# Optimization experiments

Hardware: AMD Instinct MI355X
Metric: run time of the kernel (lower is better)

Reference implementation:

```python
import jax, jax.numpy as jnp
import numpy as np

LBASE = 256
L1_BASE = LBASE // 2 + 1   # 129
LPA = 128
L1_PA = LPA + 1            # 129
L2 = 16
L2_HALF = L2 // 2          # 8
L3 = 64
LOUTPUT = L3 + LPA + LBASE // 2  # 320
MAX_PLY = 60
COUNT = 6
BUCKET_SIZE = MAX_PLY // COUNT   # 10
B = 262144


def setup_inputs() -> dict:
    key = jax.random.key(0)
    ks = jax.random.split(key, 12)
    def w(k, shape, fan_in):
        bound = 1.0 / np.sqrt(fan_in)
        return jax.random.uniform(k, shape, jnp.float32, -bound, bound)
    return {
        "x_base": jax.random.uniform(ks[0], (B, LBASE // 2), jnp.float32),
        "x_pa": jax.random.uniform(ks[1], (B, LPA), jnp.float32),
        "mobility": jax.random.uniform(ks[2], (B, 1), jnp.float32),
        "ply": jax.random.randint(ks[3], (B,), 0, MAX_PLY),
        "W1b": w(ks[4], (COUNT, L2_HALF, L1_BASE), L1_BASE),
        "b1b": w(ks[5], (COUNT, L2_HALF), L1_BASE),
        "W1pa": w(ks[6], (COUNT, L2_HALF, L1_PA), L1_PA),
        "b1pa": w(ks[7], (COUNT, L2_HALF), L1_PA),
        "W2": w(ks[8], (COUNT, L3, L2 * 2), L2 * 2),
        "b2": w(ks[9], (COUNT, L3), L2 * 2),
        "Wout": w(ks[10], (COUNT, 1, LOUTPUT), LOUTPUT),
        "bout": jnp.zeros((COUNT, 1), jnp.float32),  # bias zeroed in __init__
    }


def _stacked_linear(x, W, b, idx):
    # per-sample bucket selection: x (B,I), W (C,O,I), b (C,O), idx (B,)
    return jnp.einsum("bi,boi->bo", x, W[idx]) + b[idx]


def reference(x_base, x_pa, mobility, ply, W1b, b1b, W1pa, b1pa, W2, b2, Wout, bout):
    idx = ply // BUCKET_SIZE                                   # (B,)
    mob = jnp.minimum(mobility * (7.0 / 255.0), 1.0)           # clamp max only
    xb = jnp.concatenate([x_base, mob], axis=1)                # (B,129)
    xpa = jnp.concatenate([x_pa, mob], axis=1)                 # (B,129)
    l1 = jnp.concatenate([
        _stacked_linear(xb, W1b, b1b, idx),
        _stacked_linear(xpa, W1pa, b1pa, idx),
    ], axis=1)                                                 # (B,16)
    l1_sq = jnp.square(l1) * (255.0 / 256.0)
    l1c = jnp.clip(jnp.concatenate([l1_sq, l1], axis=1), 0.0, 1.0)  # (B,32)
    l2x = _stacked_linear(l1c, W2, b2, idx)                    # (B,64)
    l2x = jnp.square(jnp.clip(l2x, 0.0, 1.0)) * (255.0 / 256.0)
    feats = jnp.concatenate([l2x, x_base, x_pa], axis=1)       # (B,320)
    return _stacked_linear(feats, Wout, bout, idx)             # (B,1)
```

## Files before the change

kernel.cpp:

```cpp
#include <hip/hip_runtime.h>


#define NB 6
#define BT 512
#define NW (BT / 64)

typedef _Float16 h2 __attribute__((ext_vector_type(2)));
typedef _Float16 h8 __attribute__((ext_vector_type(8)));
typedef float f4 __attribute__((ext_vector_type(4)));

__device__ __forceinline__ h2 pk2(float x, float y) {
    return __builtin_bit_cast(h2, __builtin_amdgcn_cvt_pkrtz(x, y));
}

__device__ __forceinline__ h8 pack8(const float4 a, const float4 b) {
    h2 p0 = pk2(a.x, a.y), p1 = pk2(a.z, a.w);
    h2 p2 = pk2(b.x, b.y), p3 = pk2(b.z, b.w);
    h8 r;
    r[0] = p0[0]; r[1] = p0[1]; r[2] = p1[0]; r[3] = p1[1];
    r[4] = p2[0]; r[5] = p2[1]; r[6] = p3[0]; r[7] = p3[1];
    return r;
}

__device__ __forceinline__ float actv(float v) {
    float u = fminf(fmaxf(v, 0.0f), 1.0f);
    return u * u * (255.0f / 256.0f);
}

__global__ __launch_bounds__(BT, 4)
void layerstacks_mfma(const float* __restrict__ x_base,
                      const float* __restrict__ x_pa,
                      const float* __restrict__ mobility,
                      const int*   __restrict__ ply,
                      const float* __restrict__ W1b,
                      const float* __restrict__ b1b,
                      const float* __restrict__ W1pa,
                      const float* __restrict__ b1pa,
                      const float* __restrict__ W2,
                      const float* __restrict__ b2,
                      const float* __restrict__ Wout,
                      const float* __restrict__ bout,
                      float* __restrict__ out)
{
    __shared__ __align__(16) _Float16 sW1[NB][2][4][4][9][8];
    __shared__ __align__(16) _Float16 sW2[NB][4][4][16][8];
    __shared__ float sWo0[NB][64];
    __shared__ float sB2[NB][64];
    __shared__ float sB1[NB][4][8];
    __shared__ float sBout[NB];
    __shared__ float sMob[BT];
    __shared__ int   sList[BT + NB * 16];
    __shared__ __align__(16) char sL1[NW * 1280];
    __shared__ int sCnt[8], sCur[8], sTb[40];
    __shared__ int sNt;

    const int tid   = threadIdx.x;
    const int lane  = tid & 63;
    const int w     = tid >> 6;
    const int gbase = blockIdx.x * BT;

    if (tid < 8) { sCnt[tid] = 0; }

    for (int e = tid; e < NB * 2 * 4 * 4 * 9 * 8; e += BT) {
        int i = e & 7;
        int rest = e >> 3;
        int n = rest % 9;   rest /= 9;
        int kb = rest & 3;  rest >>= 2;
        int t = rest & 3;   rest >>= 2;
        int st = rest & 1;
        int b = rest >> 1;
        int k = t * 32 + kb * 8 + i;
        float v;
        if (n < 8) {
            const float* Wx = st ? W1pa : W1b;
            v = Wx[b * 1032 + n * 129 + k];
        } else {
            v = st ? Wout[b * 320 + 192 + k] : Wout[b * 320 + 64 + k];
        }
        sW1[b][st][t][kb][n][i] = (_Float16)v;
    }
    for (int e = tid; e < NB * 4 * 4 * 16 * 8; e += BT) {
        int i = e & 7;
        int j = (e >> 3) & 15;
        int kb = (e >> 7) & 3;
        int T = (e >> 9) & 3;
        int b = e >> 11;
        int n = T * 16 + j;
        int k = kb * 8 + i;
        int u = k >> 1;
        int colw = (k & 1) ? (16 + u) : u;
        sW2[b][T][kb][j][i] = (_Float16)W2[b * 2048 + n * 32 + colw];
    }
    for (int e = tid; e < NB * 64; e += BT) {
        int b = e >> 6, n = e & 63;
        sWo0[b][n] = Wout[b * 320 + n];
        sB2[b][n]  = b2[e];
    }
    if (tid < NB * 4 * 8) {
        int n = tid & 7, which = (tid >> 3) & 3, b = tid >> 5;
        float v;
        if (which == 0)      v = b1b[b * 8 + n];
        else if (which == 1) v = b1pa[b * 8 + n];
        else if (which == 2) v = W1b [b * 1032 + n * 129 + 128];
        else                 v = W1pa[b * 1032 + n * 129 + 128];
        sB1[b][which][n] = v;
    }
    if (tid < NB) sBout[tid] = bout[tid];
    sMob[tid] = fminf(mobility[gbase + tid] * (7.0f / 255.0f), 1.0f);
    for (int e = tid; e < BT + NB * 16; e += BT) sList[e] = -1;

    const int bb = ply[gbase + tid] / 10;
    __syncthreads();

    #pragma unroll
    for (int b = 0; b < NB; ++b) {
        unsigned long long mk = __ballot(bb == b);
        if (bb == b) {
            int lead = __ffsll((long long)mk) - 1;
            if (lane == lead) atomicAdd(&sCnt[b], __popcll(mk));
        }
    }
    __syncthreads();

    if (tid == 0) {
        int off = 0, tt = 0;
        for (int b = 0; b < NB; ++b) {
            sCur[b] = off;
            int ntl = (sCnt[b] + 15) >> 4;
            for (int q = 0; q < ntl; ++q) sTb[tt++] = b;
            off += ntl << 4;
        }
        sNt = tt;
    }
    __syncthreads();

    #pragma unroll
    for (int b = 0; b < NB; ++b) {
        unsigned long long mk = __ballot(bb == b);
        if (bb == b) {
            int lead = __ffsll((long long)mk) - 1;
            int pfx = __popcll(mk & ((1ull << lane) - 1ull));
            int base = 0;
            if (lane == lead) base = atomicAdd(&sCur[b], __popcll(mk));
            base = __shfl(base, lead);
            sList[base + pfx] = tid;
        }
    }
    __syncthreads();

    const int ntiles = sNt;
    const int col = lane & 15;
    const int qd  = lane >> 4;
    char* lb = sL1 + w * 1280;

    for (int tl = w; tl < ntiles; tl += NW) {
        const int bkt = sTb[tl];
        const int t16 = tl << 4;

        const int sl0 = sList[t16 + qd * 4 + 0];
        const int sl1 = sList[t16 + qd * 4 + 1];
        const int sl2 = sList[t16 + qd * 4 + 2];
        const int sl3 = sList[t16 + qd * 4 + 3];
        int sA = sList[t16 + col];
        if (sA < 0) sA = sList[t16];

        const float* xbrow = x_base + (size_t)(gbase + sA) * 128 + qd * 8;
        const float* xprow = x_pa   + (size_t)(gbase + sA) * 128 + qd * 8;

        float4 b00, b01, b10, b11, b20, b21, b30, b31;
        float4 q00, q01, q10, q11, q20, q21, q30, q31;
        asm volatile(
            "global_load_dwordx4 %0,  %[ab], off\n\t"
            "global_load_dwordx4 %1,  %[ab], off offset:16\n\t"
            "global_load_dwordx4 %2,  %[ab], off offset:128\n\t"
            "global_load_dwordx4 %3,  %[ab], off offset:144\n\t"
            "global_load_dwordx4 %4,  %[ab], off offset:256\n\t"
            "global_load_dwordx4 %5,  %[ab], off offset:272\n\t"
            "global_load_dwordx4 %6,  %[ab], off offset:384\n\t"
            "global_load_dwordx4 %7,  %[ab], off offset:400\n\t"
            "global_load_dwordx4 %8,  %[ap], off\n\t"
            "global_load_dwordx4 %9,  %[ap], off offset:16\n\t"
            "global_load_dwordx4 %10, %[ap], off offset:128\n\t"
            "global_load_dwordx4 %11, %[ap], off offset:144\n\t"
            "global_load_dwordx4 %12, %[ap], off offset:256\n\t"
            "global_load_dwordx4 %13, %[ap], off offset:272\n\t"
            "global_load_dwordx4 %14, %[ap], off offset:384\n\t"
            "global_load_dwordx4 %15, %[ap], off offset:400\n\t"
            "s_waitcnt vmcnt(0)"
            : "=v"(b00), "=v"(b01), "=v"(b10), "=v"(b11),
              "=v"(b20), "=v"(b21), "=v"(b30), "=v"(b31),
              "=v"(q00), "=v"(q01), "=v"(q10), "=v"(q11),
              "=v"(q20), "=v"(q21), "=v"(q30), "=v"(q31)
            : [ab] "v"(xbrow), [ap] "v"(xprow)
            : "memory");

        const float mob0 = (sl0 >= 0) ? sMob[sl0] : 0.0f;
        const float mob1 = (sl1 >= 0) ? sMob[sl1] : 0.0f;
        const float mob2 = (sl2 >= 0) ? sMob[sl2] : 0.0f;
        const float mob3 = (sl3 >= 0) ? sMob[sl3] : 0.0f;

        const int c7 = col & 7;
        const bool a8 = (col < 8);
        const int ncl = a8 ? col : 8;
        const float bb1 = sB1[bkt][0][c7], bp1 = sB1[bkt][1][c7];
        const float mwb = sB1[bkt][2][c7], mwp = sB1[bkt][3][c7];

        f4 cb, cp;
        cb[0] = a8 ? bb1 + mwb * mob0 : 0.0f;
        cb[1] = a8 ? bb1 + mwb * mob1 : 0.0f;
        cb[2] = a8 ? bb1 + mwb * mob2 : 0.0f;
        cb[3] = a8 ? bb1 + mwb * mob3 : 0.0f;
        cp[0] = a8 ? bp1 + mwp * mob0 : 0.0f;
        cp[1] = a8 ? bp1 + mwp * mob1 : 0.0f;
        cp[2] = a8 ? bp1 + mwp * mob2 : 0.0f;
        cp[3] = a8 ? bp1 + mwp * mob3 : 0.0f;

        const h8 wa0 = *(const h8*)&sW1[bkt][0][0][qd][ncl][0];
        const h8 wa1 = *(const h8*)&sW1[bkt][0][1][qd][ncl][0];
        const h8 wa2 = *(const h8*)&sW1[bkt][0][2][qd][ncl][0];
        const h8 wa3 = *(const h8*)&sW1[bkt][0][3][qd][ncl][0];
        const h8 wp0 = *(const h8*)&sW1[bkt][1][0][qd][ncl][0];
        const h8 wp1 = *(const h8*)&sW1[bkt][1][1][qd][ncl][0];
        const h8 wp2 = *(const h8*)&sW1[bkt][1][2][qd][ncl][0];
        const h8 wp3 = *(const h8*)&sW1[bkt][1][3][qd][ncl][0];

        cb = __builtin_amdgcn_mfma_f32_16x16x32_f16(pack8(b00, b01), wa0, cb, 0, 0, 0);
        cp = __builtin_amdgcn_mfma_f32_16x16x32_f16(pack8(q00, q01), wp0, cp, 0, 0, 0);
        cb = __builtin_amdgcn_mfma_f32_16x16x32_f16(pack8(b10, b11), wa1, cb, 0, 0, 0);
        cp = __builtin_amdgcn_mfma_f32_16x16x32_f16(pack8(q10, q11), wp1, cp, 0, 0, 0);
        cb = __builtin_amdgcn_mfma_f32_16x16x32_f16(pack8(b20, b21), wa2, cb, 0, 0, 0);
        cp = __builtin_amdgcn_mfma_f32_16x16x32_f16(pack8(q20, q21), wp2, cp, 0, 0, 0);
        cb = __builtin_amdgcn_mfma_f32_16x16x32_f16(pack8(b30, b31), wa3, cb, 0, 0, 0);
        cp = __builtin_amdgcn_mfma_f32_16x16x32_f16(pack8(q30, q31), wp3, cp, 0, 0, 0);

        if (col < 8) {
            #pragma unroll
            for (int r = 0; r < 4; ++r) {
                const int row = qd * 4 + r;
                float v = cb[r];
                *(h2*)(lb + row * 80 + col * 4) =
                    pk2(fminf(v * v * (255.0f / 256.0f), 1.0f),
                        fminf(fmaxf(v, 0.0f), 1.0f));
                v = cp[r];
                *(h2*)(lb + row * 80 + 32 + col * 4) =
                    pk2(fminf(v * v * (255.0f / 256.0f), 1.0f),
                        fminf(fmaxf(v, 0.0f), 1.0f));
            }
        } else if (col == 8) {
            #pragma unroll
            for (int r = 0; r < 4; ++r) {
                const int row = qd * 4 + r;
                *(float*)(lb + row * 80 + 64) = cb[r];
                *(float*)(lb + row * 80 + 68) = cp[r];
            }
        }

        const h8 a2 = *(const h8*)(lb + col * 80 + qd * 16);
        const float s0 = sB2[bkt][col];
        const float s1 = sB2[bkt][16 + col];
        const float s2 = sB2[bkt][32 + col];
        const float s3 = sB2[bkt][48 + col];
        f4 c20 = {s0, s0, s0, s0};
        f4 c21 = {s1, s1, s1, s1};
        f4 c22 = {s2, s2, s2, s2};
        f4 c23 = {s3, s3, s3, s3};
        c20 = __builtin_amdgcn_mfma_f32_16x16x32_f16(a2, *(const h8*)&sW2[bkt][0][qd][col][0], c20, 0, 0, 0);
        c21 = __builtin_amdgcn_mfma_f32_16x16x32_f16(a2, *(const h8*)&sW2[bkt][1][qd][col][0], c21, 0, 0, 0);
        c22 = __builtin_amdgcn_mfma_f32_16x16x32_f16(a2, *(const h8*)&sW2[bkt][2][qd][col][0], c22, 0, 0, 0);
        c23 = __builtin_amdgcn_mfma_f32_16x16x32_f16(a2, *(const h8*)&sW2[bkt][3][qd][col][0], c23, 0, 0, 0);

        const float wo0 = sWo0[bkt][col];
        const float wo1 = sWo0[bkt][16 + col];
        const float wo2 = sWo0[bkt][32 + col];
        const float wo3 = sWo0[bkt][48 + col];
        float p0 = actv(c20[0]) * wo0 + actv(c21[0]) * wo1 + actv(c22[0]) * wo2 + actv(c23[0]) * wo3;
        float p1 = actv(c20[1]) * wo0 + actv(c21[1]) * wo1 + actv(c22[1]) * wo2 + actv(c23[1]) * wo3;
        float p2 = actv(c20[2]) * wo0 + actv(c21[2]) * wo1 + actv(c22[2]) * wo2 + actv(c23[2]) * wo3;
        float p3 = actv(c20[3]) * wo0 + actv(c21[3]) * wo1 + actv(c22[3]) * wo2 + actv(c23[3]) * wo3;
        #pragma unroll
        for (int m = 1; m < 16; m <<= 1) {
            p0 += __shfl_xor(p0, m, 64);
            p1 += __shfl_xor(p1, m, 64);
            p2 += __shfl_xor(p2, m, 64);
            p3 += __shfl_xor(p3, m, 64);
        }

        if (col == 0) {
            const float bo = sBout[bkt];
            if (sl0 >= 0)
                out[gbase + sl0] = bo + *(const float*)(lb + (qd * 4 + 0) * 80 + 64)
                                      + *(const float*)(lb + (qd * 4 + 0) * 80 + 68) + p0;
            if (sl1 >= 0)
                out[gbase + sl1] = bo + *(const float*)(lb + (qd * 4 + 1) * 80 + 64)
                                      + *(const float*)(lb + (qd * 4 + 1) * 80 + 68) + p1;
            if (sl2 >= 0)
                out[gbase + sl2] = bo + *(const float*)(lb + (qd * 4 + 2) * 80 + 64)
                                      + *(const float*)(lb + (qd * 4 + 2) * 80 + 68) + p2;
            if (sl3 >= 0)
                out[gbase + sl3] = bo + *(const float*)(lb + (qd * 4 + 3) * 80 + 64)
                                      + *(const float*)(lb + (qd * 4 + 3) * 80 + 68) + p3;
        }
    }
}

extern "C" void kernel_launch(void* const* d_in, const int* in_sizes, int n_in,
                              void* d_out, int out_size, void* d_ws, size_t ws_size,
                              hipStream_t stream) {
    const float* x_base   = (const float*)d_in[0];
    const float* x_pa     = (const float*)d_in[1];
    const float* mobility = (const float*)d_in[2];
    const int*   ply      = (const int*)d_in[3];
    const float* W1b      = (const float*)d_in[4];
    const float* b1b      = (const float*)d_in[5];
    const float* W1pa     = (const float*)d_in[6];
    const float* b1pa     = (const float*)d_in[7];
    const float* W2       = (const float*)d_in[8];
    const float* b2       = (const float*)d_in[9];
    const float* Wout     = (const float*)d_in[10];
    const float* bout     = (const float*)d_in[11];
    float* out = (float*)d_out;

    const int B = in_sizes[3];
    const int blocks = B / BT;
    layerstacks_mfma<<<blocks, BT, 0, stream>>>(
        x_base, x_pa, mobility, ply, W1b, b1b, W1pa, b1pa, W2, b2, Wout, bout, out);
}
```

Baseline: 62.33 us.

## Replace per-block bucket sorting with masked per-bucket MFMA over natural tiles

Drops the ballot/atomic counting sort of samples into bucket-homogeneous tiles, along with its extra barriers and the gathered row indices. Tiles are now contiguous 16-row slices. For each bucket present in a tile, the MFMAs run with the A operand masked per row, and biases and output weights are looked up per row. This removes the sorting and synchronisation overhead and makes the row loads contiguous. The cost is up to six times more layer-1 and layer-2 MFMA work per tile when buckets are mixed, which is likely with random ply values.

After: 57.73 us. -7.4%, faster.

```diff
diff --git a/kernel.cpp b/kernel.cpp
--- a/kernel.cpp
+++ b/kernel.cpp
@@ -4,10 +4,12 @@
 #define NB 6
 #define BT 512
 #define NW (BT / 64)
+#define TILES (BT / 16)
 
 typedef _Float16 h2 __attribute__((ext_vector_type(2)));
 typedef _Float16 h8 __attribute__((ext_vector_type(8)));
 typedef float f4 __attribute__((ext_vector_type(4)));
+typedef unsigned u4v __attribute__((ext_vector_type(4)));
 
 __device__ __forceinline__ h2 pk2(float x, float y) {
     return __builtin_bit_cast(h2, __builtin_amdgcn_cvt_pkrtz(x, y));
@@ -20,6 +22,13 @@
     r[0] = p0[0]; r[1] = p0[1]; r[2] = p1[0]; r[3] = p1[1];
     r[4] = p2[0]; r[5] = p2[1]; r[6] = p3[0]; r[7] = p3[1];
     return r;
+}
+
+__device__ __forceinline__ h8 mask8(h8 v, unsigned m) {
+    u4v u = __builtin_bit_cast(u4v, v);
+    u4v mm = {m, m, m, m};
+    u &= mm;
+    return __builtin_bit_cast(h8, u);
 }
 
 __device__ __forceinline__ float actv(float v) {
@@ -49,17 +58,13 @@
     __shared__ float sB1[NB][4][8];
     __shared__ float sBout[NB];
     __shared__ float sMob[BT];
-    __shared__ int   sList[BT + NB * 16];
+    __shared__ int   sBkt[BT];
     __shared__ __align__(16) char sL1[NW * 1280];
-    __shared__ int sCnt[8], sCur[8], sTb[40];
-    __shared__ int sNt;
 
     const int tid   = threadIdx.x;
     const int lane  = tid & 63;
     const int w     = tid >> 6;
     const int gbase = blockIdx.x * BT;
-
-    if (tid < 8) { sCnt[tid] = 0; }
 
     for (int e = tid; e < NB * 2 * 4 * 4 * 9 * 8; e += BT) {
         int i = e & 7;
@@ -107,66 +112,19 @@
     }
     if (tid < NB) sBout[tid] = bout[tid];
     sMob[tid] = fminf(mobility[gbase + tid] * (7.0f / 255.0f), 1.0f);
-    for (int e = tid; e < BT + NB * 16; e += BT) sList[e] = -1;
-
-    const int bb = ply[gbase + tid] / 10;
+    sBkt[tid] = ply[gbase + tid] / 10;
     __syncthreads();
 
-    #pragma unroll
-    for (int b = 0; b < NB; ++b) {
-        unsigned long long mk = __ballot(bb == b);
-        if (bb == b) {
-            int lead = __ffsll((long long)mk) - 1;
-            if (lane == lead) atomicAdd(&sCnt[b], __popcll(mk));
-        }
-    }
-    __syncthreads();
-
-    if (tid == 0) {
-        int off = 0, tt = 0;
-        for (int b = 0; b < NB; ++b) {
-            sCur[b] = off;
-            int ntl = (sCnt[b] + 15) >> 4;
-            for (int q = 0; q < ntl; ++q) sTb[tt++] = b;
-            off += ntl << 4;
-        }
-        sNt = tt;
-    }
-    __syncthreads();
-
-    #pragma unroll
-    for (int b = 0; b < NB; ++b) {
-        unsigned long long mk = __ballot(bb == b);
-        if (bb == b) {
-            int lead = __ffsll((long long)mk) - 1;
-            int pfx = __popcll(mk & ((1ull << lane) - 1ull));
-            int base = 0;
-            if (lane == lead) base = atomicAdd(&sCur[b], __popcll(mk));
-            base = __shfl(base, lead);
-            sList[base + pfx] = tid;
-        }
-    }
-    __syncthreads();
-
-    const int ntiles = sNt;
     const int col = lane & 15;
     const int qd  = lane >> 4;
     char* lb = sL1 + w * 1280;
 
-    for (int tl = w; tl < ntiles; tl += NW) {
-        const int bkt = sTb[tl];
+    for (int tl = w; tl < TILES; tl += NW) {
         const int t16 = tl << 4;
-
-        const int sl0 = sList[t16 + qd * 4 + 0];
-        const int sl1 = sList[t16 + qd * 4 + 1];
-        const int sl2 = sList[t16 + qd * 4 + 2];
-        const int sl3 = sList[t16 + qd * 4 + 3];
-        int sA = sList[t16 + col];
-        if (sA < 0) sA = sList[t16];
-
-        const float* xbrow = x_base + (size_t)(gbase + sA) * 128 + qd * 8;
-        const float* xprow = x_pa   + (size_t)(gbase + sA) * 128 + qd * 8;
-
+        const int r0 = t16 + qd * 4;
+
+        const float* xbrow = x_base + (size_t)(gbase + t16 + col) * 128 + qd * 8;
+        const float* xprow = x_pa   + (size_t)(gbase + t16 + col) * 128 + qd * 8;
         float4 b00, b01, b10, b11, b20, b21, b30, b31;
         float4 q00, q01, q10, q11, q20, q21, q30, q31;
         asm volatile(
@@ -194,44 +152,44 @@
             : [ab] "v"(xbrow), [ap] "v"(xprow)
             : "memory");
 
-        const float mob0 = (sl0 >= 0) ? sMob[sl0] : 0.0f;
-        const float mob1 = (sl1 >= 0) ? sMob[sl1] : 0.0f;
-        const float mob2 = (sl2 >= 0) ? sMob[sl2] : 0.0f;
-        const float mob3 = (sl3 >= 0) ? sMob[sl3] : 0.0f;
+        const h8 xa0 = pack8(b00, b01), xa1 = pack8(b10, b11);
+        const h8 xa2 = pack8(b20, b21), xa3 = pack8(b30, b31);
+        const h8 xp0 = pack8(q00, q01), xp1 = pack8(q10, q11);
+        const h8 xp2 = pack8(q20, q21), xp3 = pack8(q30, q31);
+
+        const int bbA = sBkt[t16 + col];
+        const int bk0 = sBkt[r0 + 0], bk1 = sBkt[r0 + 1];
+        const int bk2 = sBkt[r0 + 2], bk3 = sBkt[r0 + 3];
+        const float m0 = sMob[r0 + 0], m1 = sMob[r0 + 1];
+        const float m2 = sMob[r0 + 2], m3 = sMob[r0 + 3];
 
         const int c7 = col & 7;
         const bool a8 = (col < 8);
         const int ncl = a8 ? col : 8;
-        const float bb1 = sB1[bkt][0][c7], bp1 = sB1[bkt][1][c7];
-        const float mwb = sB1[bkt][2][c7], mwp = sB1[bkt][3][c7];
 
         f4 cb, cp;
-        cb[0] = a8 ? bb1 + mwb * mob0 : 0.0f;
-        cb[1] = a8 ? bb1 + mwb * mob1 : 0.0f;
-        cb[2] = a8 ? bb1 + mwb * mob2 : 0.0f;
-        cb[3] = a8 ? bb1 + mwb * mob3 : 0.0f;
-        cp[0] = a8 ? bp1 + mwp * mob0 : 0.0f;
-        cp[1] = a8 ? bp1 + mwp * mob1 : 0.0f;
-        cp[2] = a8 ? bp1 + mwp * mob2 : 0.0f;
-        cp[3] = a8 ? bp1 + mwp * mob3 : 0.0f;
-
-        const h8 wa0 = *(const h8*)&sW1[bkt][0][0][qd][ncl][0];
-        const h8 wa1 = *(const h8*)&sW1[bkt][0][1][qd][ncl][0];
-        const h8 wa2 = *(const h8*)&sW1[bkt][0][2][qd][ncl][0];
-        const h8 wa3 = *(const h8*)&sW1[bkt][0][3][qd][ncl][0];
-        const h8 wp0 = *(const h8*)&sW1[bkt][1][0][qd][ncl][0];
-        const h8 wp1 = *(const h8*)&sW1[bkt][1][1][qd][ncl][0];
-        const h8 wp2 = *(const h8*)&sW1[bkt][1][2][qd][ncl][0];
-        const h8 wp3 = *(const h8*)&sW1[bkt][1][3][qd][ncl][0];
-
-        cb = __builtin_amdgcn_mfma_f32_16x16x32_f16(pack8(b00, b01), wa0, cb, 0, 0, 0);
-        cp = __builtin_amdgcn_mfma_f32_16x16x32_f16(pack8(q00, q01), wp0, cp, 0, 0, 0);
-        cb = __builtin_amdgcn_mfma_f32_16x16x32_f16(pack8(b10, b11), wa1, cb, 0, 0, 0);
-        cp = __builtin_amdgcn_mfma_f32_16x16x32_f16(pack8(q10, q11), wp1, cp, 0, 0, 0);
-        cb = __builtin_amdgcn_mfma_f32_16x16x32_f16(pack8(b20, b21), wa2, cb, 0, 0, 0);
-        cp = __builtin_amdgcn_mfma_f32_16x16x32_f16(pack8(q20, q21), wp2, cp, 0, 0, 0);
-        cb = __builtin_amdgcn_mfma_f32_16x16x32_f16(pack8(b30, b31), wa3, cb, 0, 0, 0);
-        cp = __builtin_amdgcn_mfma_f32_16x16x32_f16(pack8(q30, q31), wp3, cp, 0, 0, 0);
+        cb[0] = a8 ? sB1[bk0][0][c7] + sB1[bk0][2][c7] * m0 : 0.0f;
+        cb[1] = a8 ? sB1[bk1][0][c7] + sB1[bk1][2][c7] * m1 : 0.0f;
+        cb[2] = a8 ? sB1[bk2][0][c7] + sB1[bk2][2][c7] * m2 : 0.0f;
+        cb[3] = a8 ? sB1[bk3][0][c7] + sB1[bk3][2][c7] * m3 : 0.0f;
+        cp[0] = a8 ? sB1[bk0][1][c7] + sB1[bk0][3][c7] * m0 : 0.0f;
+        cp[1] = a8 ? sB1[bk1][1][c7] + sB1[bk1][3][c7] * m1 : 0.0f;
+        cp[2] = a8 ? sB1[bk2][1][c7] + sB1[bk2][3][c7] * m2 : 0.0f;
+        cp[3] = a8 ? sB1[bk3][1][c7] + sB1[bk3][3][c7] * m3 : 0.0f;
+
+        #pragma unroll
+        for (int b = 0; b < NB; ++b) {
+            if (!__any(bbA == b)) continue;
+            const unsigned mA = (bbA == b) ? 0xFFFFFFFFu : 0u;
+            cb = __builtin_amdgcn_mfma_f32_16x16x32_f16(mask8(xa0, mA), *(const h8*)&sW1[b][0][0][qd][ncl][0], cb, 0, 0, 0);
+            cp = __builtin_amdgcn_mfma_f32_16x16x32_f16(mask8(xp0, mA), *(const h8*)&sW1[b][1][0][qd][ncl][0], cp, 0, 0, 0);
+            cb = __builtin_amdgcn_mfma_f32_16x16x32_f16(mask8(xa1, mA), *(const h8*)&sW1[b][0][1][qd][ncl][0], cb, 0, 0, 0);
+            cp = __builtin_amdgcn_mfma_f32_16x16x32_f16(mask8(xp1, mA), *(const h8*)&sW1[b][1][1][qd][ncl][0], cp, 0, 0, 0);
+            cb = __builtin_amdgcn_mfma_f32_16x16x32_f16(mask8(xa2, mA), *(const h8*)&sW1[b][0][2][qd][ncl][0], cb, 0, 0, 0);
+            cp = __builtin_amdgcn_mfma_f32_16x16x32_f16(mask8(xp2, mA), *(const h8*)&sW1[b][1][2][qd][ncl][0], cp, 0, 0, 0);
+            cb = __builtin_amdgcn_mfma_f32_16x16x32_f16(mask8(xa3, mA), *(const h8*)&sW1[b][0][3][qd][ncl][0], cb, 0, 0, 0);
+            cp = __builtin_amdgcn_mfma_f32_16x16x32_f16(mask8(xp3, mA), *(const h8*)&sW1[b][1][3][qd][ncl][0], cp, 0, 0, 0);
+        }
 
         if (col < 8) {
             #pragma unroll
@@ -256,27 +214,35 @@
         }
 
         const h8 a2 = *(const h8*)(lb + col * 80 + qd * 16);
-        const float s0 = sB2[bkt][col];
-        const float s1 = sB2[bkt][16 + col];
-        const float s2 = sB2[bkt][32 + col];
-        const float s3 = sB2[bkt][48 + col];
-        f4 c20 = {s0, s0, s0, s0};
-        f4 c21 = {s1, s1, s1, s1};
-        f4 c22 = {s2, s2, s2, s2};
-        f4 c23 = {s3, s3, s3, s3};
-        c20 = __builtin_amdgcn_mfma_f32_16x16x32_f16(a2, *(const h8*)&sW2[bkt][0][qd][col][0], c20, 0, 0, 0);
-        c21 = __builtin_amdgcn_mfma_f32_16x16x32_f16(a2, *(const h8*)&sW2[bkt][1][qd][col][0], c21, 0, 0, 0);
-        c22 = __builtin_amdgcn_mfma_f32_16x16x32_f16(a2, *(const h8*)&sW2[bkt][2][qd][col][0], c22, 0, 0, 0);
-        c23 = __builtin_amdgcn_mfma_f32_16x16x32_f16(a2, *(const h8*)&sW2[bkt][3][qd][col][0], c23, 0, 0, 0);
-
-        const float wo0 = sWo0[bkt][col];
-        const float wo1 = sWo0[bkt][16 + col];
-        const float wo2 = sWo0[bkt][32 + col];
-        const float wo3 = sWo0[bkt][48 + col];
-        float p0 = actv(c20[0]) * wo0 + actv(c21[0]) * wo1 + actv(c22[0]) * wo2 + actv(c23[0]) * wo3;
-        float p1 = actv(c20[1]) * wo0 + actv(c21[1]) * wo1 + actv(c22[1]) * wo2 + actv(c23[1]) * wo3;
-        float p2 = actv(c20[2]) * wo0 + actv(c21[2]) * wo1 + actv(c22[2]) * wo2 + actv(c23[2]) * wo3;
-        float p3 = actv(c20[3]) * wo0 + actv(c21[3]) * wo1 + actv(c22[3]) * wo2 + actv(c23[3]) * wo3;
+        f4 c20, c21, c22, c23;
+        c20[0] = sB2[bk0][col];      c20[1] = sB2[bk1][col];
+        c20[2] = sB2[bk2][col];      c20[3] = sB2[bk3][col];
+        c21[0] = sB2[bk0][16 + col]; c21[1] = sB2[bk1][16 + col];
+        c21[2] = sB2[bk2][16 + col]; c21[3] = sB2[bk3][16 + col];
+        c22[0] = sB2[bk0][32 + col]; c22[1] = sB2[bk1][32 + col];
+        c22[2] = sB2[bk2][32 + col]; c22[3] = sB2[bk3][32 + col];
+        c23[0] = sB2[bk0][48 + col]; c23[1] = sB2[bk1][48 + col];
+        c23[2] = sB2[bk2][48 + col]; c23[3] = sB2[bk3][48 + col];
+
+        #pragma unroll
+        for (int b = 0; b < NB; ++b) {
+            if (!__any(bbA == b)) continue;
+            const unsigned mA = (bbA == b) ? 0xFFFFFFFFu : 0u;
+            const h8 a2m = mask8(a2, mA);
+            c20 = __builtin_amdgcn_mfma_f32_16x16x32_f16(a2m, *(const h8*)&sW2[b][0][qd][col][0], c20, 0, 0, 0);
+            c21 = __builtin_amdgcn_mfma_f32_16x16x32_f16(a2m, *(const h8*)&sW2[b][1][qd][col][0], c21, 0, 0, 0);
+            c22 = __builtin_amdgcn_mfma_f32_16x16x32_f16(a2m, *(const h8*)&sW2[b][2][qd][col][0], c22, 0, 0, 0);
+            c23 = __builtin_amdgcn_mfma_f32_16x16x32_f16(a2m, *(const h8*)&sW2[b][3][qd][col][0], c23, 0, 0, 0);
+        }
+
+        float p0 = actv(c20[0]) * sWo0[bk0][col]      + actv(c21[0]) * sWo0[bk0][16 + col]
+                 + actv(c22[0]) * sWo0[bk0][32 + col] + actv(c23[0]) * sWo0[bk0][48 + col];
+        float p1 = actv(c20[1]) * sWo0[bk1][col]      + actv(c21[1]) * sWo0[bk1][16 + col]
+                 + actv(c22[1]) * sWo0[bk1][32 + col] + actv(c23[1]) * sWo0[bk1][48 + col];
+        float p2 = actv(c20[2]) * sWo0[bk2][col]      + actv(c21[2]) * sWo0[bk2][16 + col]
+                 + actv(c22[2]) * sWo0[bk2][32 + col] + actv(c23[2]) * sWo0[bk2][48 + col];
+        float p3 = actv(c20[3]) * sWo0[bk3][col]      + actv(c21[3]) * sWo0[bk3][16 + col]
+                 + actv(c22[3]) * sWo0[bk3][32 + col] + actv(c23[3]) * sWo0[bk3][48 + col];
         #pragma unroll
         for (int m = 1; m < 16; m <<= 1) {
             p0 += __shfl_xor(p0, m, 64);
@@ -286,19 +252,18 @@
         }
 
         if (col == 0) {
-            const float bo = sBout[bkt];
-            if (sl0 >= 0)
-                out[gbase + sl0] = bo + *(const float*)(lb + (qd * 4 + 0) * 80 + 64)
-                                      + *(const float*)(lb + (qd * 4 + 0) * 80 + 68) + p0;
-            if (sl1 >= 0)
-                out[gbase + sl1] = bo + *(const float*)(lb + (qd * 4 + 1) * 80 + 64)
-                                      + *(const float*)(lb + (qd * 4 + 1) * 80 + 68) + p1;
-            if (sl2 >= 0)
-                out[gbase + sl2] = bo + *(const float*)(lb + (qd * 4 + 2) * 80 + 64)
-                                      + *(const float*)(lb + (qd * 4 + 2) * 80 + 68) + p2;
-            if (sl3 >= 0)
-                out[gbase + sl3] = bo + *(const float*)(lb + (qd * 4 + 3) * 80 + 64)
-                                      + *(const float*)(lb + (qd * 4 + 3) * 80 + 68) + p3;
+            out[gbase + r0 + 0] = sBout[bk0]
+                + *(const float*)(lb + (qd * 4 + 0) * 80 + 64)
+                + *(const float*)(lb + (qd * 4 + 0) * 80 + 68) + p0;
+            out[gbase + r0 + 1] = sBout[bk1]
+                + *(const float*)(lb + (qd * 4 + 1) * 80 + 64)
+                + *(const float*)(lb + (qd * 4 + 1) * 80 + 68) + p1;
+            out[gbase + r0 + 2] = sBout[bk2]
+                + *(const float*)(lb + (qd * 4 + 2) * 80 + 64)
+                + *(const float*)(lb + (qd * 4 + 2) * 80 + 68) + p2;
+            out[gbase + r0 + 3] = sBout[bk3]
+                + *(const float*)(lb + (qd * 4 + 3) * 80 + 64)
+                + *(const float*)(lb + (qd * 4 + 3) * 80 + 68) + p3;
         }
     }
 }
```
